# Performance work log

Measured on AMD Instinct MI355X. Metric: run time of the kernel, lower is better.

The kernel has to match this reference:

```python
import jax, jax.numpy as jnp
import numpy as np

B, H, D = 16, 16, 128          # batch (decode seqs), heads, head_dim
BLK = 16                        # paged-KV block size (hard-coded in source)
MAXB = 128                      # blocks per sequence
MAXS = MAXB * BLK               # 2048 max context
NBLK = B * MAXB                 # total cache blocks
SOFTMAX_SCALE = 1.0 / np.sqrt(D)


def setup_inputs() -> dict:
    key = jax.random.key(0)
    ks = jax.random.split(key, 8)
    Q = jax.random.normal(ks[0], (B, H, D), dtype=jnp.float32)
    K = jax.random.normal(ks[1], (B, H, D), dtype=jnp.float32)
    V = jax.random.normal(ks[2], (B, H, D), dtype=jnp.float32)
    Kcache = jax.random.normal(ks[3], (NBLK, BLK, H, D), dtype=jnp.float32)
    Vcache = jax.random.normal(ks[4], (NBLK, BLK, H, D), dtype=jnp.float32)
    # context length per sequence (includes the new decode token)
    input_length = jax.random.randint(ks[5], (B,), 1, MAXS + 1).astype(jnp.int32)
    # each sequence owns a contiguous run of blocks
    block_tables = jnp.arange(B * MAXB, dtype=jnp.int32).reshape(B, MAXB)
    # flat slot index where the new token's K/V are written
    pos = input_length - 1
    save_slots = (block_tables[jnp.arange(B), pos // BLK] * BLK + pos % BLK).astype(jnp.int64)
    # per-token RoPE cos/sin
    ang = jax.random.uniform(ks[6], (B, D), dtype=jnp.float32) * (2.0 * np.pi)
    cos, sin = jnp.cos(ang), jnp.sin(ang)
    mask = jnp.zeros((B, MAXS), dtype=jnp.float32)  # additive attention bias
    return {"Q": Q, "K": K, "V": V, "Kcache": Kcache, "Vcache": Vcache,
            "cos": cos, "sin": sin, "mask": mask,
            "input_length": input_length, "save_slots": save_slots,
            "block_tables": block_tables, "max_s": MAXS}


def _rope(x, cos, sin):
    # LLaMA rotate-half RoPE; cos/sin are [B,1,D], x is [B,H,D]
    d2 = x.shape[-1] // 2
    x1, x2 = x[..., :d2], x[..., d2:]
    rot = jnp.concatenate([-x2, x1], axis=-1)
    return x * cos + rot * sin


def reference(Q, K, V, Kcache, Vcache, cos, sin, mask,
              input_length, save_slots, block_tables, max_s):
    c = cos[:, None, :]
    s = sin[:, None, :]
    qr = _rope(Q, c, s)                      # [B,H,D]
    kr = _rope(K, c, s)                      # [B,H,D]
    # scatter new token K/V into the paged cache (flat slot view)
    Kf = Kcache.reshape(-1, H, D).at[save_slots].set(kr)
    Vf = Vcache.reshape(-1, H, D).at[save_slots].set(V)
    # gather each sequence's context slots via its block table
    slot_idx = (block_tables[:, :, None] * BLK
                + jnp.arange(BLK, dtype=jnp.int32)).reshape(B, MAXS)  # [B,S]
    keys = Kf[slot_idx]                      # [B,S,H,D]
    vals = Vf[slot_idx]                      # [B,S,H,D]
    scores = jnp.einsum('bhd,bshd->bhs', qr, keys) * SOFTMAX_SCALE + mask[:, None, :]
    valid = jnp.arange(MAXS, dtype=jnp.int32)[None, :] < input_length[:, None]
    scores = jnp.where(valid[:, None, :], scores, jnp.float32(-1e30))
    p = jax.nn.softmax(scores, axis=-1)
    out = jnp.einsum('bhs,bshd->bhd', p, vals)  # [B,H,D]
    return out
```

## Files before the change

### kernel.cpp

```cpp
#include <hip/hip_runtime.h>
#include <hip/hip_bf16.h>

#define BATCH 16
#define NHEAD 16
#define DHEAD 128
#define BLK   16
#define MAXB  128
#define MAXS  (MAXB * BLK)
#define NSPLIT 8
#define CHUNK  (MAXS / NSPLIT)
#define SCALE  0.0883883476483184f

#define WSQ_FLOATS (BATCH * NHEAD * DHEAD)
#define PART_STRIDE (DHEAD + 2)

__global__ void rope_scatter(const float* __restrict__ Q,
                             const float* __restrict__ K,
                             const float* __restrict__ V,
                             float* __restrict__ Kcache,
                             float* __restrict__ Vcache,
                             const float* __restrict__ cosb,
                             const float* __restrict__ sinb,
                             const int* __restrict__ save_slots,
                             float* __restrict__ ws_q) {
    const int bh = blockIdx.x;
    const int b  = bh / NHEAD;
    const int h  = bh % NHEAD;
    const int d  = threadIdx.x;

    const float c = cosb[b * DHEAD + d];
    const float s = sinb[b * DHEAD + d];

    const size_t qidx = (size_t)bh * DHEAD + d;
    const float qv = Q[qidx];
    const float qrot = (d < DHEAD / 2) ? -Q[qidx + DHEAD / 2] : Q[qidx - DHEAD / 2];
    ws_q[qidx] = qv * c + qrot * s;

    const float kv = K[qidx];
    const float krot = (d < DHEAD / 2) ? -K[qidx + DHEAD / 2] : K[qidx - DHEAD / 2];
    const float kr = kv * c + krot * s;

    const int slot = save_slots[b];
    const size_t cidx = (size_t)slot * (NHEAD * DHEAD) + (size_t)h * DHEAD + d;
    Kcache[cidx] = kr;
    Vcache[cidx] = V[qidx];
}

__global__ __launch_bounds__(256) void attn_partial(
        const float* __restrict__ Kcache,
        const float* __restrict__ Vcache,
        const float* __restrict__ mask,
        const int* __restrict__ input_length,
        const int* __restrict__ block_tables,
        const float* __restrict__ ws_q,
        float* __restrict__ ws_part) {
    const int split = blockIdx.x;
    const int h     = blockIdx.y;
    const int b     = blockIdx.z;
    const int tid   = threadIdx.x;
    const int hw    = tid >> 5;
    const int ln    = tid & 31;

    __shared__ int   sbase[CHUNK];
    __shared__ float sp[CHUNK];
    __shared__ float sred[8];
    __shared__ float sacc[8][DHEAD];

    float* part = ws_part + ((size_t)((b * NHEAD + h) * NSPLIT + split)) * PART_STRIDE;

    const int L  = input_length[b];
    const int s0 = split * CHUNK;
    if (s0 >= L) {
        if (tid < DHEAD) part[tid] = 0.0f;
        if (tid == 0) { part[DHEAD] = -1e30f; part[DHEAD + 1] = 0.0f; }
        return;
    }
    const int n = min(CHUNK, L - s0);

    if (tid < n) {
        const int s = s0 + tid;
        sbase[tid] = block_tables[b * MAXB + (s >> 4)] * (BLK * NHEAD * DHEAD)
                   + (s & (BLK - 1)) * (NHEAD * DHEAD) + h * DHEAD;
    }
    const float4 q = ((const float4*)(ws_q + (size_t)(b * NHEAD + h) * DHEAD))[ln];
    __syncthreads();

    #pragma unroll 4
    for (int i = hw; i < n; i += 8) {
        const float4 k = ((const float4*)(Kcache + sbase[i]))[ln];
        float d = k.x * q.x + k.y * q.y + k.z * q.z + k.w * q.w;
        #pragma unroll
        for (int off = 16; off >= 1; off >>= 1)
            d += __shfl_xor(d, off, 64);
        if (ln == 0) sp[i] = d;
    }
    __syncthreads();

    const float sc = (tid < n) ? sp[tid] * SCALE + mask[(size_t)b * MAXS + s0 + tid]
                               : -1e30f;
    float wm = sc;
    #pragma unroll
    for (int off = 32; off >= 1; off >>= 1)
        wm = fmaxf(wm, __shfl_xor(wm, off, 64));
    if ((tid & 63) == 0) sred[tid >> 6] = wm;
    __syncthreads();
    const float M = fmaxf(fmaxf(sred[0], sred[1]), fmaxf(sred[2], sred[3]));
    const float p = (tid < n) ? __expf(sc - M) : 0.0f;
    sp[tid] = p;
    float wsum = p;
    #pragma unroll
    for (int off = 32; off >= 1; off >>= 1)
        wsum += __shfl_xor(wsum, off, 64);
    if ((tid & 63) == 0) sred[4 + (tid >> 6)] = wsum;
    __syncthreads();
    const float l = (sred[4] + sred[5]) + (sred[6] + sred[7]);

    float4 acc = make_float4(0.0f, 0.0f, 0.0f, 0.0f);
    #pragma unroll 4
    for (int i = hw; i < n; i += 8) {
        const float4 v = ((const float4*)(Vcache + sbase[i]))[ln];
        const float pi = sp[i];
        acc.x += pi * v.x;
        acc.y += pi * v.y;
        acc.z += pi * v.z;
        acc.w += pi * v.w;
    }

    ((float4*)sacc[hw])[ln] = acc;
    __syncthreads();
    if (tid < DHEAD) {
        float a = 0.0f;
        #pragma unroll
        for (int w = 0; w < 8; ++w) a += sacc[w][tid];
        part[tid] = a;
        if (tid == 0) { part[DHEAD] = M; part[DHEAD + 1] = l; }
    }
}

__global__ void attn_combine(const float* __restrict__ ws_part,
                             float* __restrict__ out) {
    const int bh = blockIdx.x;
    const int d  = threadIdx.x;

    const float* base = ws_part + (size_t)bh * NSPLIT * PART_STRIDE;

    float M = -1e30f;
    #pragma unroll
    for (int s = 0; s < NSPLIT; ++s)
        M = fmaxf(M, base[s * PART_STRIDE + DHEAD]);

    float lsum = 0.0f, a = 0.0f;
    #pragma unroll
    for (int s = 0; s < NSPLIT; ++s) {
        const float f = __expf(base[s * PART_STRIDE + DHEAD] - M);
        lsum += base[s * PART_STRIDE + DHEAD + 1] * f;
        a    += base[s * PART_STRIDE + d] * f;
    }
    out[(size_t)bh * DHEAD + d] = a / lsum;
}

extern "C" void kernel_launch(void* const* d_in, const int* in_sizes, int n_in,
                              void* d_out, int out_size, void* d_ws, size_t ws_size,
                              hipStream_t stream) {
    const float* Q       = (const float*)d_in[0];
    const float* K       = (const float*)d_in[1];
    const float* V       = (const float*)d_in[2];
    float*       Kcache  = (float*)d_in[3];
    float*       Vcache  = (float*)d_in[4];
    const float* cosb    = (const float*)d_in[5];
    const float* sinb    = (const float*)d_in[6];
    const float* mask    = (const float*)d_in[7];
    const int*   in_len  = (const int*)d_in[8];
    const int*   slots   = (const int*)d_in[9];
    const int*   btab    = (const int*)d_in[10];

    float* ws_q    = (float*)d_ws;
    float* ws_part = ws_q + WSQ_FLOATS;
    float* out     = (float*)d_out;

    rope_scatter<<<BATCH * NHEAD, DHEAD, 0, stream>>>(
        Q, K, V, Kcache, Vcache, cosb, sinb, slots, ws_q);

    dim3 grid2(NSPLIT, NHEAD, BATCH);
    attn_partial<<<grid2, 256, 0, stream>>>(
        Kcache, Vcache, mask, in_len, btab, ws_q, ws_part);

    attn_combine<<<BATCH * NHEAD, DHEAD, 0, stream>>>(ws_part, out);
}
```

Baseline: 472.3 us.

## Replace fixed split grid with atomic work queue over valid chunks

Adds an init kernel that builds a compact list of only the (batch, split, head) work items that hold valid tokens, and turns attn_partial into a persistent-style loop that pulls items through an atomic counter. The combine kernel now reads only the valid splits for each sequence. This removes launching and scheduling blocks that would exit early, at the cost of an extra kernel launch, an atomic and a barrier per item, and the grid still launches 2048 blocks, many of which exit at once.

```diff
diff --git a/kernel.cpp b/kernel.cpp
--- a/kernel.cpp
+++ b/kernel.cpp
@@ -13,6 +13,7 @@
 
 #define WSQ_FLOATS (BATCH * NHEAD * DHEAD)
 #define PART_STRIDE (DHEAD + 2)
+#define WSPART_FLOATS (BATCH * NHEAD * NSPLIT * PART_STRIDE)
 
 __global__ void rope_scatter(const float* __restrict__ Q,
                              const float* __restrict__ K,
@@ -46,6 +47,24 @@
     Vcache[cidx] = V[qidx];
 }
 
+__global__ void init_queue(const int* __restrict__ input_length,
+                           int* __restrict__ qmeta,
+                           int* __restrict__ items) {
+    const int t   = threadIdx.x;
+    const int myb = t >> 4;
+    const int myh = t & 15;
+    int mypre = 0, myc = 0, tot = 0;
+    for (int b = 0; b < BATCH; ++b) {
+        const int c = (input_length[b] + CHUNK - 1) / CHUNK;
+        if (b < myb)  mypre += c;
+        if (b == myb) myc = c;
+        tot += c;
+    }
+    for (int s = 0; s < myc; ++s)
+        items[(mypre + s) * NHEAD + myh] = (myb << 16) | (s << 8) | myh;
+    if (t == 0) { qmeta[0] = 0; qmeta[1] = tot * NHEAD; }
+}
+
 __global__ __launch_bounds__(256) void attn_partial(
         const float* __restrict__ Kcache,
         const float* __restrict__ Vcache,
@@ -53,105 +72,114 @@
         const int* __restrict__ input_length,
         const int* __restrict__ block_tables,
         const float* __restrict__ ws_q,
+        int* __restrict__ qmeta,
+        const int* __restrict__ items,
         float* __restrict__ ws_part) {
-    const int split = blockIdx.x;
-    const int h     = blockIdx.y;
-    const int b     = blockIdx.z;
-    const int tid   = threadIdx.x;
-    const int hw    = tid >> 5;
-    const int ln    = tid & 31;
-
+    const int tid = threadIdx.x;
+    const int hw  = tid >> 5;
+    const int ln  = tid & 31;
+
+    __shared__ int   s_item;
     __shared__ int   sbase[CHUNK];
     __shared__ float sp[CHUNK];
     __shared__ float sred[8];
     __shared__ float sacc[8][DHEAD];
 
-    float* part = ws_part + ((size_t)((b * NHEAD + h) * NSPLIT + split)) * PART_STRIDE;
-
-    const int L  = input_length[b];
-    const int s0 = split * CHUNK;
-    if (s0 >= L) {
-        if (tid < DHEAD) part[tid] = 0.0f;
-        if (tid == 0) { part[DHEAD] = -1e30f; part[DHEAD + 1] = 0.0f; }
-        return;
+    const int n_items = qmeta[1];
+
+    for (;;) {
+        if (tid == 0) s_item = atomicAdd(&qmeta[0], 1);
+        __syncthreads();
+        const int it = s_item;
+        if (it >= n_items) return;
+        const int item  = items[it];
+        const int b     = item >> 16;
+        const int split = (item >> 8) & 255;
+        const int h     = item & 255;
+
+        const int L  = input_length[b];
+        const int s0 = split * CHUNK;
+        const int n  = min(CHUNK, L - s0);
+
+        if (tid < n) {
+            const int s = s0 + tid;
+            sbase[tid] = block_tables[b * MAXB + (s >> 4)] * (BLK * NHEAD * DHEAD)
+                       + (s & (BLK - 1)) * (NHEAD * DHEAD) + h * DHEAD;
+        }
+        const float4 q = ((const float4*)(ws_q + (size_t)(b * NHEAD + h) * DHEAD))[ln];
+        __syncthreads();
+
+        #pragma unroll 4
+        for (int i = hw; i < n; i += 8) {
+            const float4 k = ((const float4*)(Kcache + sbase[i]))[ln];
+            float d = k.x * q.x + k.y * q.y + k.z * q.z + k.w * q.w;
+            #pragma unroll
+            for (int off = 16; off >= 1; off >>= 1)
+                d += __shfl_xor(d, off, 64);
+            if (ln == 0) sp[i] = d;
+        }
+        __syncthreads();
+
+        const float sc = (tid < n) ? sp[tid] * SCALE + mask[(size_t)b * MAXS + s0 + tid]
+                                   : -1e30f;
+        float wm = sc;
+        #pragma unroll
+        for (int off = 32; off >= 1; off >>= 1)
+            wm = fmaxf(wm, __shfl_xor(wm, off, 64));
+        if ((tid & 63) == 0) sred[tid >> 6] = wm;
+        __syncthreads();
+        const float M = fmaxf(fmaxf(sred[0], sred[1]), fmaxf(sred[2], sred[3]));
+        const float p = (tid < n) ? __expf(sc - M) : 0.0f;
+        sp[tid] = p;
+        float wsum = p;
+        #pragma unroll
+        for (int off = 32; off >= 1; off >>= 1)
+            wsum += __shfl_xor(wsum, off, 64);
+        if ((tid & 63) == 0) sred[4 + (tid >> 6)] = wsum;
+        __syncthreads();
+        const float l = (sred[4] + sred[5]) + (sred[6] + sred[7]);
+
+        float4 acc = make_float4(0.0f, 0.0f, 0.0f, 0.0f);
+        #pragma unroll 4
+        for (int i = hw; i < n; i += 8) {
+            const float4 v = ((const float4*)(Vcache + sbase[i]))[ln];
+            const float pi = sp[i];
+            acc.x += pi * v.x;
+            acc.y += pi * v.y;
+            acc.z += pi * v.z;
+            acc.w += pi * v.w;
+        }
+
+        ((float4*)sacc[hw])[ln] = acc;
+        __syncthreads();
+        float* part = ws_part + ((size_t)((b * NHEAD + h) * NSPLIT + split)) * PART_STRIDE;
+        if (tid < DHEAD) {
+            float a = 0.0f;
+            #pragma unroll
+            for (int w = 0; w < 8; ++w) a += sacc[w][tid];
+            part[tid] = a;
+            if (tid == 0) { part[DHEAD] = M; part[DHEAD + 1] = l; }
+        }
+        __syncthreads();
     }
-    const int n = min(CHUNK, L - s0);
-
-    if (tid < n) {
-        const int s = s0 + tid;
-        sbase[tid] = block_tables[b * MAXB + (s >> 4)] * (BLK * NHEAD * DHEAD)
-                   + (s & (BLK - 1)) * (NHEAD * DHEAD) + h * DHEAD;
-    }
-    const float4 q = ((const float4*)(ws_q + (size_t)(b * NHEAD + h) * DHEAD))[ln];
-    __syncthreads();
-
-    #pragma unroll 4
-    for (int i = hw; i < n; i += 8) {
-        const float4 k = ((const float4*)(Kcache + sbase[i]))[ln];
-        float d = k.x * q.x + k.y * q.y + k.z * q.z + k.w * q.w;
-        #pragma unroll
-        for (int off = 16; off >= 1; off >>= 1)
-            d += __shfl_xor(d, off, 64);
-        if (ln == 0) sp[i] = d;
-    }
-    __syncthreads();
-
-    const float sc = (tid < n) ? sp[tid] * SCALE + mask[(size_t)b * MAXS + s0 + tid]
-                               : -1e30f;
-    float wm = sc;
-    #pragma unroll
-    for (int off = 32; off >= 1; off >>= 1)
-        wm = fmaxf(wm, __shfl_xor(wm, off, 64));
-    if ((tid & 63) == 0) sred[tid >> 6] = wm;
-    __syncthreads();
-    const float M = fmaxf(fmaxf(sred[0], sred[1]), fmaxf(sred[2], sred[3]));
-    const float p = (tid < n) ? __expf(sc - M) : 0.0f;
-    sp[tid] = p;
-    float wsum = p;
-    #pragma unroll
-    for (int off = 32; off >= 1; off >>= 1)
-        wsum += __shfl_xor(wsum, off, 64);
-    if ((tid & 63) == 0) sred[4 + (tid >> 6)] = wsum;
-    __syncthreads();
-    const float l = (sred[4] + sred[5]) + (sred[6] + sred[7]);
-
-    float4 acc = make_float4(0.0f, 0.0f, 0.0f, 0.0f);
-    #pragma unroll 4
-    for (int i = hw; i < n; i += 8) {
-        const float4 v = ((const float4*)(Vcache + sbase[i]))[ln];
-        const float pi = sp[i];
-        acc.x += pi * v.x;
-        acc.y += pi * v.y;
-        acc.z += pi * v.z;
-        acc.w += pi * v.w;
-    }
-
-    ((float4*)sacc[hw])[ln] = acc;
-    __syncthreads();
-    if (tid < DHEAD) {
-        float a = 0.0f;
-        #pragma unroll
-        for (int w = 0; w < 8; ++w) a += sacc[w][tid];
-        part[tid] = a;
-        if (tid == 0) { part[DHEAD] = M; part[DHEAD + 1] = l; }
-    }
 }
 
 __global__ void attn_combine(const float* __restrict__ ws_part,
+                             const int* __restrict__ input_length,
                              float* __restrict__ out) {
     const int bh = blockIdx.x;
+    const int b  = bh >> 4;
     const int d  = threadIdx.x;
 
+    const int ns = (input_length[b] + CHUNK - 1) / CHUNK;
     const float* base = ws_part + (size_t)bh * NSPLIT * PART_STRIDE;
 
     float M = -1e30f;
-    #pragma unroll
-    for (int s = 0; s < NSPLIT; ++s)
+    for (int s = 0; s < ns; ++s)
         M = fmaxf(M, base[s * PART_STRIDE + DHEAD]);
 
     float lsum = 0.0f, a = 0.0f;
-    #pragma unroll
-    for (int s = 0; s < NSPLIT; ++s) {
+    for (int s = 0; s < ns; ++s) {
         const float f = __expf(base[s * PART_STRIDE + DHEAD] - M);
         lsum += base[s * PART_STRIDE + DHEAD + 1] * f;
         a    += base[s * PART_STRIDE + d] * f;
@@ -176,14 +204,17 @@
 
     float* ws_q    = (float*)d_ws;
     float* ws_part = ws_q + WSQ_FLOATS;
+    int*   qmeta   = (int*)(ws_part + WSPART_FLOATS);
+    int*   qitems  = qmeta + 2;
     float* out     = (float*)d_out;
 
     rope_scatter<<<BATCH * NHEAD, DHEAD, 0, stream>>>(
         Q, K, V, Kcache, Vcache, cosb, sinb, slots, ws_q);
 
-    dim3 grid2(NSPLIT, NHEAD, BATCH);
-    attn_partial<<<grid2, 256, 0, stream>>>(
-        Kcache, Vcache, mask, in_len, btab, ws_q, ws_part);
-
-    attn_combine<<<BATCH * NHEAD, DHEAD, 0, stream>>>(ws_part, out);
-}
+    init_queue<<<1, 256, 0, stream>>>(in_len, qmeta, qitems);
+
+    attn_partial<<<2048, 256, 0, stream>>>(
+        Kcache, Vcache, mask, in_len, btab, ws_q, qmeta, qitems, ws_part);
+
+    attn_combine<<<BATCH * NHEAD, DHEAD, 0, stream>>>(ws_part, in_len, out);
+}
```

After: 504.2 us. 6.7% more time.
